# Optimization experiments

Measured on AMD Instinct MI355X. Metric: run time of the kernel, lower is better.

Reference implementation:

```python
import jax, jax.numpy as jnp
import numpy as np

EPS = 1e-10
BIG = 1e10

def setup_inputs() -> dict:
    key = jax.random.key(0)
    ks = jax.random.split(key, 8)
    B, N, D, H = 8, 2048, 128, 128
    K = 1434  # ceil(0.7 * N)
    X = jax.random.normal(ks[0], (B, N, D), dtype=jnp.float32)
    adj = jax.random.uniform(ks[1], (B, N, N), dtype=jnp.float32)
    mask = jnp.ones((B, N), dtype=jnp.float32)
    top_index = jax.random.randint(ks[2], (B, K), 0, N)
    # GCN params (xavier-normal-ish weights, zero bias)
    W1 = jax.random.normal(ks[3], (D, H), dtype=jnp.float32) * np.sqrt(2.0 / (D + H))
    b1 = jnp.zeros((H,), dtype=jnp.float32)
    W2 = jax.random.normal(ks[4], (H, H), dtype=jnp.float32) * np.sqrt(2.0 / (H + H))
    b2 = jnp.zeros((H,), dtype=jnp.float32)
    w_b = jax.random.uniform(ks[5], (1, H, 1), dtype=jnp.float32, minval=-1.0, maxval=1.0)
    tau = jnp.asarray(1.0, dtype=jnp.float32)
    return {"X": X, "adj": adj, "mask": mask, "W1": W1, "b1": b1,
            "W2": W2, "b2": b2, "w_b": w_b, "tau": tau, "top_index": top_index}

def reference(X, adj, mask, W1, b1, W2, b2, w_b, tau, top_index):
    # --- stacked GCN layers: relu((adj @ x) @ W + b) ---
    h = jax.nn.relu(jnp.matmul(jnp.matmul(adj, X), W1) + b1)
    h = jax.nn.relu(jnp.matmul(jnp.matmul(adj, h), W2) + b2)
    hidden = mask[:, :, None] * h  # [B,N,H]

    # --- neighbor-softmax attention (softmax == 'neibor') ---
    att_b = jnp.matmul(hidden, w_b)[..., 0] + (mask - 1.0) * BIG  # [B,N]
    att_b = jnp.exp((att_b - jnp.max(att_b, axis=1, keepdims=True)) * jnp.abs(tau))
    denom = jnp.einsum('bnm,bm->bn', adj, att_b) + EPS  # khop=1
    diag = jnp.diagonal(adj, axis1=1, axis2=2)  # [B,N]
    att_b = att_b * diag / denom
    att_b = att_b * jnp.sum(adj, axis=1)  # dnorm, adj_norm='none'
    att = att_b * mask

    Z = att[:, :, None] * hidden  # [B,N,H]

    # --- pooling via sampled top_index (full mask => k_list[i]==k_max) ---
    assign_m = jnp.take_along_axis(adj, top_index[:, :, None], axis=1)  # [B,K,N]
    assign_m = assign_m / (jnp.sum(assign_m, axis=1, keepdims=True) + EPS)
    H_out = jnp.matmul(assign_m, Z)  # [B,K,H]
    new_adj = jnp.matmul(jnp.matmul(assign_m, adj), jnp.swapaxes(assign_m, 1, 2))  # [B,K,K]
    new_mask = jnp.ones((X.shape[0], top_index.shape[1]), dtype=X.dtype)

    # mean pool readout
    out = jnp.sum(mask[:, :, None] * hidden, axis=1) / jnp.sum(mask, axis=1, keepdims=True)
    return out, H_out, new_adj, new_mask
```

## Files before the change

### kernel.cpp

```cpp
#include <hip/hip_runtime.h>
#include <hip/hip_bf16.h>

namespace {

constexpr int Bb = 8;
constexpr int Nn = 2048;
constexpr int Hh = 128;
constexpr int Kp = 1434;
constexpr int KpPad = 1536;
constexpr float kEps = 1e-10f;
constexpr float kBig = 1e10f;

using bf16x8 = __attribute__((ext_vector_type(8))) short;
using f32x4  = __attribute__((ext_vector_type(4))) float;

__device__ __forceinline__ float bf2f(unsigned u) {
  union { float f; unsigned q; } x; x.q = u << 16; return x.f;
}

__device__ __forceinline__ unsigned short f2bfbits(float f) {
  __hip_bfloat16 h = __float2bfloat16(f);
  return *reinterpret_cast<unsigned short*>(&h);
}

template<typename TA>
__device__ __forceinline__ void load8(const TA* p, float v[8]) {
  const float4* q = reinterpret_cast<const float4*>(p);
  float4 x0 = q[0], x1 = q[1];
  v[0]=x0.x; v[1]=x0.y; v[2]=x0.z; v[3]=x0.w;
  v[4]=x1.x; v[5]=x1.y; v[6]=x1.z; v[7]=x1.w;
}

template<typename TC>
__device__ __forceinline__ TC cvt_out(float v) {
  if constexpr (sizeof(TC) == 2) {
    return __float2bfloat16(v);
  } else {
    return v;
  }
}

__device__ __forceinline__ void gload_lds16(const void* g, void* l) {
  __builtin_amdgcn_global_load_lds(
      (const __attribute__((address_space(1))) void*)g,
      (__attribute__((address_space(3))) void*)l, 16, 0, 0);
}

template<typename TC>
__global__ __launch_bounds__(256, 4)
void mgemm_k(const __hip_bfloat16* __restrict__ A, long lda, long sA,
             const __hip_bfloat16* __restrict__ Bt, long ldb, long sB,
             const int* __restrict__ ag, int ag_stride, int Mg,
             const int* __restrict__ bg, int bg_stride, int Ng,
             TC* __restrict__ C, long ldc, long sC,
             int Ms, int Ns, int Kd)
{
  __shared__ char smem[32768];
  char* smA = smem;
  char* smB = smem + 16384;
  const int t = threadIdx.x;

  const int gx = gridDim.x, gy = gridDim.y;
  const int nwg = gx * gy * (int)gridDim.z;
  int lin = ((int)blockIdx.z * gy + (int)blockIdx.y) * gx + (int)blockIdx.x;
  lin = (lin & 7) * (nwg >> 3) + (lin >> 3);
  const int bx = lin % gx;
  const int by = (lin / gx) % gy;
  const int b  = lin / (gx * gy);

  const int m0 = by * 128, n0 = bx * 128;
  const int lane = t & 63, w = t >> 6;
  const int wr = w >> 1, wc = w & 1;

  const __hip_bfloat16* Ab = A + (size_t)b * sA;
  const __hip_bfloat16* Bb_ = Bt + (size_t)b * sB;

  const int srow = t >> 3;
  const int scol = ((t & 7) ^ (srow & 7)) * 16;
  const char* gA[4]; const char* gB[4];
#pragma unroll
  for (int q = 0; q < 4; ++q) {
    const int rowq = q * 32 + srow;
    long ga = m0 + rowq;
    if (ag) ga = (ga < Mg) ? (long)ag[(size_t)b * ag_stride + ga] : 0;
    gA[q] = (const char*)(Ab + ga * lda) + scol;
    long gb = n0 + rowq;
    if (bg) gb = (gb < Ng) ? (long)bg[(size_t)b * bg_stride + gb] : 0;
    gB[q] = (const char*)(Bb_ + gb * ldb) + scol;
  }

  f32x4 acc[4][4] = {};
  const int fr = lane & 15, kg = lane >> 4, fx = lane & 7;

  for (int kk = 0; kk < Kd; kk += 64) {
    __syncthreads();
#pragma unroll
    for (int q = 0; q < 4; ++q) {
      gload_lds16(gA[q] + (size_t)kk * 2, smA + q * 4096 + t * 16);
      gload_lds16(gB[q] + (size_t)kk * 2, smB + q * 4096 + t * 16);
    }
    __syncthreads();
#pragma unroll
    for (int ks = 0; ks < 2; ++ks) {
      bf16x8 aF[4], bF[4];
      const int slotbase = kg | (ks << 2);
#pragma unroll
      for (int mi = 0; mi < 4; ++mi) {
        const int off = (wr * 64 + mi * 16 + fr) * 128 + ((slotbase ^ fx) << 4);
        aF[mi] = *(const bf16x8*)(smA + off);
      }
#pragma unroll
      for (int ni = 0; ni < 4; ++ni) {
        const int off = (wc * 64 + ni * 16 + fr) * 128 + ((slotbase ^ fx) << 4);
        bF[ni] = *(const bf16x8*)(smB + off);
      }
#pragma unroll
      for (int mi = 0; mi < 4; ++mi)
#pragma unroll
        for (int ni = 0; ni < 4; ++ni)
          acc[mi][ni] = __builtin_amdgcn_mfma_f32_16x16x32_bf16(
              aF[mi], bF[ni], acc[mi][ni], 0, 0, 0);
    }
  }

  const int crow0 = m0 + wr * 64 + (lane >> 4) * 4;
  const int ccol0 = n0 + wc * 64 + fr;
#pragma unroll
  for (int mi = 0; mi < 4; ++mi) {
#pragma unroll
    for (int r = 0; r < 4; ++r) {
      const int row = crow0 + mi * 16 + r;
      if (row >= Ms) continue;
#pragma unroll
      for (int ni = 0; ni < 4; ++ni) {
        const int col = ccol0 + ni * 16;
        if (col >= Ns) continue;
        C[(size_t)b * sC + (size_t)row * ldc + col] = cvt_out<TC>(acc[mi][ni][r]);
      }
    }
  }
}

template<bool GATHER>
__global__ __launch_bounds__(256, 3)
void mlayer2_k(const __hip_bfloat16* __restrict__ A, long lda, long sA,
               const __hip_bfloat16* __restrict__ Bhi,
               const __hip_bfloat16* __restrict__ Blo, long ldb, long sB,
               const int* __restrict__ ag, int ag_stride, int Mg,
               float* __restrict__ P, int Mpad, int Kchunk)
{
  __shared__ char smem[49152];
  char* smA   = smem;
  char* smBhi = smem + 16384;
  char* smBlo = smem + 32768;
  const int t = threadIdx.x;
  const int b = blockIdx.z;
  const int sk = blockIdx.x;
  const int m0 = blockIdx.y * 128;
  const int k0 = sk * Kchunk;
  const int lane = t & 63, w = t >> 6;
  const int wr = w >> 1, wc = w & 1;

  const int srow = t >> 3;
  const int scol = ((t & 7) ^ (srow & 7)) * 16;
  const char* gA[4]; const char* gBhi[4]; const char* gBlo[4];
#pragma unroll
  for (int q = 0; q < 4; ++q) {
    const int rowq = q * 32 + srow;
    long ga = m0 + rowq;
    if (GATHER) ga = (ga < Mg) ? (long)ag[(size_t)b * ag_stride + ga] : 0;
    gA[q]   = (const char*)(A + (size_t)b * sA + ga * lda + k0) + scol;
    gBhi[q] = (const char*)(Bhi + (size_t)b * sB + (size_t)rowq * ldb + k0) + scol;
    gBlo[q] = (const char*)(Blo + (size_t)b * sB + (size_t)rowq * ldb + k0) + scol;
  }

  f32x4 acc[4][4] = {};
  const int fr = lane & 15, kg = lane >> 4, fx = lane & 7;

  for (int ks = 0; ks < Kchunk; ks += 64) {
    __syncthreads();
#pragma unroll
    for (int q = 0; q < 4; ++q) {
      gload_lds16(gA[q]   + (size_t)ks * 2, smA   + q * 4096 + t * 16);
      gload_lds16(gBhi[q] + (size_t)ks * 2, smBhi + q * 4096 + t * 16);
      gload_lds16(gBlo[q] + (size_t)ks * 2, smBlo + q * 4096 + t * 16);
    }
    __syncthreads();
#pragma unroll
    for (int ks2 = 0; ks2 < 2; ++ks2) {
      bf16x8 aF[4];
      const int slotbase = kg | (ks2 << 2);
#pragma unroll
      for (int mi = 0; mi < 4; ++mi) {
        const int off = (wr * 64 + mi * 16 + fr) * 128 + ((slotbase ^ fx) << 4);
        aF[mi] = *(const bf16x8*)(smA + off);
      }
#pragma unroll
      for (int ni = 0; ni < 4; ++ni) {
        const int off = (wc * 64 + ni * 16 + fr) * 128 + ((slotbase ^ fx) << 4);
        const bf16x8 bhi = *(const bf16x8*)(smBhi + off);
        const bf16x8 blo = *(const bf16x8*)(smBlo + off);
#pragma unroll
        for (int mi = 0; mi < 4; ++mi) {
          acc[mi][ni] = __builtin_amdgcn_mfma_f32_16x16x32_bf16(aF[mi], bhi, acc[mi][ni], 0, 0, 0);
          acc[mi][ni] = __builtin_amdgcn_mfma_f32_16x16x32_bf16(aF[mi], blo, acc[mi][ni], 0, 0, 0);
        }
      }
    }
  }

  float* Pp = P + ((size_t)sk * Bb + b) * Mpad * 128;
  const int crow0 = m0 + wr * 64 + (lane >> 4) * 4;
  const int ccol0 = wc * 64 + fr;
#pragma unroll
  for (int mi = 0; mi < 4; ++mi)
#pragma unroll
    for (int r = 0; r < 4; ++r) {
      const int row = crow0 + mi * 16 + r;
#pragma unroll
      for (int ni = 0; ni < 4; ++ni)
        Pp[(size_t)row * 128 + ccol0 + ni * 16] = acc[mi][ni][r];
    }
}

template<bool MASKED>
__global__ __launch_bounds__(256)
void red_layer_k(const float* __restrict__ P, const float* __restrict__ bias,
                 const float* __restrict__ mask, float* __restrict__ out)
{
  const size_t o = ((size_t)blockIdx.x * 256 + threadIdx.x) * 4;
  const size_t stride = (size_t)Bb * Nn * Hh;
  float4 s = {0.f, 0.f, 0.f, 0.f};
#pragma unroll
  for (int sk = 0; sk < 8; ++sk) {
    const float4 v = *(const float4*)(P + sk * stride + o);
    s.x += v.x; s.y += v.y; s.z += v.z; s.w += v.w;
  }
  const int h = (int)(o & 127);
  const float4 bi = *(const float4*)(bias + h);
  s.x = fmaxf(s.x + bi.x, 0.f);
  s.y = fmaxf(s.y + bi.y, 0.f);
  s.z = fmaxf(s.z + bi.z, 0.f);
  s.w = fmaxf(s.w + bi.w, 0.f);
  if (MASKED) {
    const int n = (int)((o >> 7) & (Nn - 1));
    const int b = (int)(o >> 18);
    const float m = mask[b * Nn + n];
    s.x *= m; s.y *= m; s.z *= m; s.w *= m;
  }
  *(float4*)(out + o) = s;
}

__global__ __launch_bounds__(128)
void red_hout_k(const float* __restrict__ P, float* __restrict__ Hout)
{
  const int k = blockIdx.x, b = blockIdx.y, h = threadIdx.x;
  const size_t stride = (size_t)Bb * KpPad * Hh;
  float s = 0.f;
#pragma unroll
  for (int sk = 0; sk < 8; ++sk)
    s += P[sk * stride + ((size_t)b * KpPad + k) * 128 + h];
  Hout[((size_t)b * Kp + k) * 128 + h] = s;
}

__global__ __launch_bounds__(256)
void wgemm_k(const float* __restrict__ A, long sA,
             const float* __restrict__ W,
             float* __restrict__ Cp)
{
  __shared__ float As[16][128];
  __shared__ float Bs[16][128];
  const int tid = threadIdx.x;
  const int p = blockIdx.x;
  const int b = blockIdx.z;
  const int m0 = blockIdx.y * 128;
  const int k0 = p * 64;
  const int ty = tid >> 4, tx = tid & 15;

  const float* Ab = A + (size_t)b * sA;

  float acc[8][8];
#pragma unroll
  for (int r = 0; r < 8; ++r)
#pragma unroll
    for (int c = 0; c < 8; ++c) acc[r][c] = 0.f;

  const int ai = tid >> 1;
  const int ak0 = (tid & 1) * 8;

  for (int kk0 = k0; kk0 < k0 + 64; kk0 += 16) {
    float av[8];
    load8<float>(Ab + (size_t)(m0 + ai) * Hh + kk0 + ak0, av);
    float bv[8];
    const int bk_row = tid >> 4, bj0 = (tid & 15) * 8;
    load8<float>(W + (size_t)(kk0 + bk_row) * Hh + bj0, bv);

    __syncthreads();
#pragma unroll
    for (int e = 0; e < 8; ++e) Bs[bk_row][bj0 + e] = bv[e];
#pragma unroll
    for (int e = 0; e < 8; ++e) As[ak0 + e][ai] = av[e];
    __syncthreads();

#pragma unroll
    for (int k = 0; k < 16; ++k) {
      const float4 a0 = *reinterpret_cast<const float4*>(&As[k][4 * ty]);
      const float4 a1 = *reinterpret_cast<const float4*>(&As[k][64 + 4 * ty]);
      const float4 b0 = *reinterpret_cast<const float4*>(&Bs[k][4 * tx]);
      const float4 b1 = *reinterpret_cast<const float4*>(&Bs[k][64 + 4 * tx]);
      const float ar[8] = {a0.x, a0.y, a0.z, a0.w, a1.x, a1.y, a1.z, a1.w};
      const float br[8] = {b0.x, b0.y, b0.z, b0.w, b1.x, b1.y, b1.z, b1.w};
#pragma unroll
      for (int r = 0; r < 8; ++r)
#pragma unroll
        for (int c = 0; c < 8; ++c)
          acc[r][c] = fmaf(ar[r], br[c], acc[r][c]);
    }
  }

  float* Cb = Cp + (size_t)p * Bb * Nn * Hh + (size_t)b * sA;
#pragma unroll
  for (int r = 0; r < 8; ++r) {
    const int gi = m0 + ((r < 4) ? (4 * ty + r) : (64 + 4 * ty + r - 4));
#pragma unroll
    for (int c = 0; c < 8; ++c) {
      const int gj = (c < 4) ? (4 * tx + c) : (64 + 4 * tx + c - 4);
      Cb[(size_t)gi * Hh + gj] = acc[r][c];
    }
  }
}


__global__ __launch_bounds__(256)
void prep_k(const float* __restrict__ adj, const float* __restrict__ invc,
            __hip_bfloat16* __restrict__ S, __hip_bfloat16* __restrict__ At,
            float* __restrict__ pa)
{
  __shared__ float tile[32][36];
  const int b = blockIdx.z;
  const long j0 = (long)blockIdx.x * 32;
  const long ibase = (long)blockIdx.y * 64;
  const int r = threadIdx.x >> 3, c4 = (threadIdx.x & 7) * 4;
  const float4 ic = *(const float4*)(invc + (size_t)b * Nn + j0 + c4);
  float cs = 0.f;
#pragma unroll
  for (int st = 0; st < 2; ++st) {
    const long i0 = ibase + st * 32;
    const float4 v = *(const float4*)(adj + ((size_t)b * Nn + (i0 + r)) * Nn + j0 + c4);
    ushort4 sv;
    sv.x = f2bfbits(v.x * ic.x);
    sv.y = f2bfbits(v.y * ic.y);
    sv.z = f2bfbits(v.z * ic.z);
    sv.w = f2bfbits(v.w * ic.w);
    *(ushort4*)((unsigned short*)S + ((size_t)b * Nn + (i0 + r)) * Nn + j0 + c4) = sv;
    tile[r][c4 + 0] = v.x;
    tile[r][c4 + 1] = v.y;
    tile[r][c4 + 2] = v.z;
    tile[r][c4 + 3] = v.w;
    __syncthreads();
    ushort4 tv;
    tv.x = f2bfbits(tile[c4 + 0][r]);
    tv.y = f2bfbits(tile[c4 + 1][r]);
    tv.z = f2bfbits(tile[c4 + 2][r]);
    tv.w = f2bfbits(tile[c4 + 3][r]);
    *(ushort4*)((unsigned short*)At + ((size_t)b * Nn + (j0 + r)) * Nn + i0 + c4) = tv;
    if (threadIdx.x < 32) {
      float a = 0.f;
#pragma unroll
      for (int rr = 0; rr < 32; ++rr) a += tile[rr][threadIdx.x];
      cs += a;
    }
    __syncthreads();
  }
  if (threadIdx.x < 32)
    pa[(((size_t)b * 32 + blockIdx.y) << 11) + j0 + threadIdx.x] = cs;
}

__global__ __launch_bounds__(256)
void tconv2_k(const float* __restrict__ p0, const float* __restrict__ p1,
              long ld_src, long s_src,
              const float* __restrict__ scale, long scale_stride,
              __hip_bfloat16* __restrict__ dst, __hip_bfloat16* __restrict__ dlo,
              long ld_dst, long s_dst)
{
  __shared__ float tile[32][36];
  const int b = blockIdx.z;
  const long i0 = (long)blockIdx.y * 32, j0 = (long)blockIdx.x * 32;
  const int r = threadIdx.x >> 3, c4 = (threadIdx.x & 7) * 4;
  const size_t soff = (size_t)b * s_src + (i0 + r) * ld_src + j0 + c4;
  float4 v = *(const float4*)(p0 + soff);
  if (p1) {
    const float4 u = *(const float4*)(p1 + soff);
    v.x += u.x; v.y += u.y; v.z += u.z; v.w += u.w;
  }
  const float sc = scale[(size_t)b * scale_stride + i0 + r];
  tile[r][c4 + 0] = v.x * sc;
  tile[r][c4 + 1] = v.y * sc;
  tile[r][c4 + 2] = v.z * sc;
  tile[r][c4 + 3] = v.w * sc;
  __syncthreads();
  float t0 = tile[c4 + 0][r], t1 = tile[c4 + 1][r], t2 = tile[c4 + 2][r], t3 = tile[c4 + 3][r];
  ushort4 hi;
  hi.x = f2bfbits(t0); hi.y = f2bfbits(t1); hi.z = f2bfbits(t2); hi.w = f2bfbits(t3);
  const size_t doff = (size_t)b * s_dst + (j0 + r) * ld_dst + i0 + c4;
  *(ushort4*)((unsigned short*)dst + doff) = hi;
  ushort4 lo;
  lo.x = f2bfbits(t0 - bf2f(hi.x));
  lo.y = f2bfbits(t1 - bf2f(hi.y));
  lo.z = f2bfbits(t2 - bf2f(hi.z));
  lo.w = f2bfbits(t3 - bf2f(hi.w));
  *(ushort4*)((unsigned short*)dlo + doff) = lo;
}


__global__ __launch_bounds__(256)
void colsum_c_part_k(const float* __restrict__ adj, const int* __restrict__ top,
                     float* __restrict__ pc)
{
  __shared__ int rows[180];
  const int b = blockIdx.z, ch = blockIdx.y;
  const int n = blockIdx.x * 256 + threadIdx.x;
  const int k0 = ch * 180;
  const int cnt = min(Kp - k0, 180);
  for (int k = threadIdx.x; k < cnt; k += 256) rows[k] = top[b * Kp + k0 + k];
  __syncthreads();
  const float* ab = adj + (size_t)b * Nn * Nn;
  float a0 = 0.f, a1 = 0.f, a2 = 0.f, a3 = 0.f;
  int k = 0;
  for (; k + 4 <= cnt; k += 4) {
    a0 += ab[(size_t)rows[k + 0] * Nn + n];
    a1 += ab[(size_t)rows[k + 1] * Nn + n];
    a2 += ab[(size_t)rows[k + 2] * Nn + n];
    a3 += ab[(size_t)rows[k + 3] * Nn + n];
  }
  for (; k < cnt; ++k) a0 += ab[(size_t)rows[k] * Nn + n];
  pc[(((size_t)b * 8 + ch) << 11) + n] = (a0 + a1) + (a2 + a3);
}

__global__ __launch_bounds__(256)
void invc_fin_k(const float* __restrict__ pc, float* __restrict__ invc,
                float* __restrict__ cvec)
{
  const int i = blockIdx.x * 256 + threadIdx.x;
  const int b = i >> 11, n = i & (Nn - 1);
  float s = 0.f;
#pragma unroll
  for (int ch = 0; ch < 8; ++ch) s += pc[(((size_t)b * 8 + ch) << 11) + n];
  const float c = s + kEps;
  cvec[i] = c;
  invc[i] = 1.f / c;
}

__global__ __launch_bounds__(256)
void csum_fin_k(const float* __restrict__ pa, float* __restrict__ csum)
{
  const int i = blockIdx.x * 256 + threadIdx.x;
  const int b = i >> 11, m = i & (Nn - 1);
  float s = 0.f;
#pragma unroll
  for (int ch = 0; ch < 32; ++ch) s += pa[(((size_t)b * 32 + ch) << 11) + m];
  csum[i] = s;
}

__global__ __launch_bounds__(256)
void denom2_k(const __hip_bfloat16* __restrict__ S, const float* __restrict__ ca,
              const float* __restrict__ cvec,
              float* __restrict__ denom, float* __restrict__ diag)
{
  const int b = blockIdx.y;
  const int w = threadIdx.x >> 6, lane = threadIdx.x & 63;
  const int n = blockIdx.x * 4 + w;
  const unsigned short* srow = (const unsigned short*)S + ((size_t)b * Nn + n) * Nn;
  const float* cap = ca + (size_t)b * Nn;
  float acc = 0.f;
#pragma unroll
  for (int j = 0; j < 4; ++j) {
    const int o = j * 512 + lane * 8;
    const uint4 u = *(const uint4*)(srow + o);
    const float4 c0 = *(const float4*)(cap + o);
    const float4 c1 = *(const float4*)(cap + o + 4);
    acc += bf2f(u.x & 0xffffu) * c0.x + bf2f(u.x >> 16) * c0.y
         + bf2f(u.y & 0xffffu) * c0.z + bf2f(u.y >> 16) * c0.w
         + bf2f(u.z & 0xffffu) * c1.x + bf2f(u.z >> 16) * c1.y
         + bf2f(u.w & 0xffffu) * c1.z + bf2f(u.w >> 16) * c1.w;
  }
#pragma unroll
  for (int o = 32; o; o >>= 1) acc += __shfl_down(acc, o, 64);
  if (lane == 0) {
    denom[(size_t)b * Nn + n] = acc;
    diag[(size_t)b * Nn + n] = bf2f(srow[n]) * cvec[(size_t)b * Nn + n];
  }
}

__global__ __launch_bounds__(128)
void readout_part_k(const float* __restrict__ hid, const float* __restrict__ mask,
                    float* __restrict__ rp)
{
  const int b = blockIdx.y, ch = blockIdx.x, h = threadIdx.x;
  const float* hp = hid + ((size_t)b * Nn + ch * 128) * Hh;
  const float* mp = mask + (size_t)b * Nn + ch * 128;
  float acc = 0.f;
#pragma unroll 1
  for (int r = 0; r < 128; ++r) acc += mp[r] * hp[(size_t)r * Hh + h];
  rp[(((size_t)b * 16 + ch) << 7) + h] = acc;
}

__global__ __launch_bounds__(128)
void readout_fin_k(const float* __restrict__ rp, const float* __restrict__ mask,
                   float* __restrict__ out)
{
  __shared__ float sm[128];
  const int b = blockIdx.x, h = threadIdx.x;
  float acc = 0.f;
#pragma unroll
  for (int ch = 0; ch < 16; ++ch) acc += rp[(((size_t)b * 16 + ch) << 7) + h];
  float ms = 0.f;
#pragma unroll
  for (int j = 0; j < 16; ++j) ms += mask[(size_t)b * Nn + h * 16 + j];
  sm[h] = ms;
  __syncthreads();
  for (int o = 64; o; o >>= 1) {
    if (h < o) sm[h] += sm[h + o];
    __syncthreads();
  }
  out[(size_t)b * Hh + h] = acc / sm[0];
}


__global__ __launch_bounds__(256)
void scores_k(const float* __restrict__ hidden, const float* __restrict__ wb,
              const float* __restrict__ mask, float* __restrict__ s)
{
  const int wid = threadIdx.x >> 6, lane = threadIdx.x & 63;
  const int row = blockIdx.x * 4 + wid;
  const float* hp = hidden + (size_t)row * Hh;
  float acc = hp[lane] * wb[lane] + hp[64 + lane] * wb[64 + lane];
#pragma unroll
  for (int o = 32; o; o >>= 1) acc += __shfl_down(acc, o, 64);
  if (lane == 0) s[row] = acc + (mask[row] - 1.f) * kBig;
}

__global__ __launch_bounds__(256)
void rowmax_k(const float* __restrict__ s, float* __restrict__ rmax)
{
  __shared__ float red[256];
  const int b = blockIdx.x;
  float m = -3.4e38f;
  for (int n = threadIdx.x; n < Nn; n += 256) m = fmaxf(m, s[b * Nn + n]);
  red[threadIdx.x] = m;
  __syncthreads();
  for (int o = 128; o; o >>= 1) {
    if (threadIdx.x < o) red[threadIdx.x] = fmaxf(red[threadIdx.x], red[threadIdx.x + o]);
    __syncthreads();
  }
  if (threadIdx.x == 0) rmax[b] = red[0];
}

__global__ __launch_bounds__(256)
void attexp_k(const float* __restrict__ s, const float* __restrict__ rmax,
              const float* __restrict__ tau, const float* __restrict__ cvec,
              float* __restrict__ atte, float* __restrict__ ca)
{
  const int i = blockIdx.x * 256 + threadIdx.x;
  const int b = i >> 11;
  const float e = expf((s[i] - rmax[b]) * fabsf(*tau));
  atte[i] = e;
  ca[i] = e * cvec[i];
}

__global__ __launch_bounds__(256)
void att_final_k(const float* __restrict__ atte, const float* __restrict__ diag,
                 const float* __restrict__ denom, const float* __restrict__ colsum,
                 const float* __restrict__ mask, float* __restrict__ att)
{
  const int i = blockIdx.x * 256 + threadIdx.x;
  att[i] = atte[i] * diag[i] / (denom[i] + kEps) * colsum[i] * mask[i];
}

__global__ __launch_bounds__(256)
void ones_k(float* __restrict__ p, int n)
{
  const int i = blockIdx.x * 256 + threadIdx.x;
  if (i < n) p[i] = 1.f;
}

}

extern "C" void kernel_launch(void* const* d_in, const int* in_sizes, int n_in,
                              void* d_out, int out_size, void* d_ws, size_t ws_size,
                              hipStream_t stream) {
  const float* X    = (const float*)d_in[0];
  const float* adj  = (const float*)d_in[1];
  const float* mask = (const float*)d_in[2];
  const float* W1   = (const float*)d_in[3];
  const float* b1   = (const float*)d_in[4];
  const float* W2   = (const float*)d_in[5];
  const float* b2   = (const float*)d_in[6];
  const float* wb   = (const float*)d_in[7];
  const float* tau  = (const float*)d_in[8];
  const int*   top  = (const int*)d_in[9];
  float* out = (float*)d_out;

  float* ws    = (float*)d_ws;
  float* h1hid = ws;
  float* Btf   = ws + 2097152;
  float* invc  = ws + 4194304;
  float* cvec  = ws + 4210688;
  float* s     = ws + 4227072;
  float* atte  = ws + 4243456;
  float* den   = ws + 4259840;
  float* diag  = ws + 4276224;
  float* csum  = ws + 4292608;
  float* att   = ws + 4308992;
  float* ca    = ws + 4325376;
  float* rmax  = ws + 4341760;
  float* pc    = ws + 4342016;
  float* pa    = ws + 4473088;
  float* rp    = ws + 4997376;
  __hip_bfloat16* S   = (__hip_bfloat16*)(ws + 5013760);
  __hip_bfloat16* At  = S + (size_t)Bb * Nn * Nn;
  float*          P   = (float*)At;
  __hip_bfloat16* T   = At + (size_t)Bb * Nn * Nn;
  float*          Tpart = (float*)T;
  if (ws_size < 204604416u) return;

  __hip_bfloat16* Bthi = (__hip_bfloat16*)Btf;
  __hip_bfloat16* Btlo = Bthi + (size_t)Bb * Hh * Nn;

  float* Hout    = out + 1024;
  float* newadj  = out + 1469440;
  float* newmask = out + 17920288;

  const long sAdj = (long)Nn * Nn;
  const long sNH  = (long)Nn * Hh;
  const long sHN  = (long)Hh * Nn;
  const long sT   = (long)KpPad * Nn;
  const long sNew = (long)Kp * Kp;

  colsum_c_part_k<<<dim3(Nn / 256, 8, Bb), 256, 0, stream>>>(adj, top, pc);
  invc_fin_k<<<dim3(Bb * Nn / 256), 256, 0, stream>>>(pc, invc, cvec);

  prep_k<<<dim3(Nn / 32, Nn / 64, Bb), 256, 0, stream>>>(adj, invc, S, At, pa);
  csum_fin_k<<<dim3(Bb * Nn / 256), 256, 0, stream>>>(pa, csum);

  mgemm_k<__hip_bfloat16><<<dim3(Nn / 128, KpPad / 128, Bb), 256, 0, stream>>>(
      S, Nn, sAdj, At, Nn, sAdj, top, Kp, Kp, nullptr, 0, 0,
      T, Nn, sT, KpPad, Nn, Nn);
  mgemm_k<float><<<dim3(KpPad / 128, KpPad / 128, Bb), 256, 0, stream>>>(
      T, Nn, sT, S, Nn, sAdj, nullptr, 0, 0, top, Kp, Kp,
      newadj, Kp, sNew, Kp, Kp, Nn);

  wgemm_k<<<dim3(2, Nn / 128, Bb), 256, 0, stream>>>(X, sNH, W1, Tpart);
  tconv2_k<<<dim3(Hh / 32, Nn / 32, Bb), 256, 0, stream>>>(
      Tpart, Tpart + (size_t)Bb * Nn * Hh, Hh, sNH, cvec, Nn, Bthi, Btlo, Nn, sHN);
  mlayer2_k<false><<<dim3(8, Nn / 128, Bb), 256, 0, stream>>>(
      S, Nn, sAdj, Bthi, Btlo, Nn, sHN, nullptr, 0, 0, P, Nn, Nn / 8);
  red_layer_k<false><<<dim3(2048), 256, 0, stream>>>(P, b1, nullptr, h1hid);

  wgemm_k<<<dim3(2, Nn / 128, Bb), 256, 0, stream>>>(h1hid, sNH, W2, Tpart);
  tconv2_k<<<dim3(Hh / 32, Nn / 32, Bb), 256, 0, stream>>>(
      Tpart, Tpart + (size_t)Bb * Nn * Hh, Hh, sNH, cvec, Nn, Bthi, Btlo, Nn, sHN);
  mlayer2_k<false><<<dim3(8, Nn / 128, Bb), 256, 0, stream>>>(
      S, Nn, sAdj, Bthi, Btlo, Nn, sHN, nullptr, 0, 0, P, Nn, Nn / 8);
  red_layer_k<true><<<dim3(2048), 256, 0, stream>>>(P, b2, mask, h1hid);

  scores_k<<<dim3(Bb * Nn / 4), 256, 0, stream>>>(h1hid, wb, mask, s);
  rowmax_k<<<dim3(Bb), 256, 0, stream>>>(s, rmax);
  attexp_k<<<dim3(Bb * Nn / 256), 256, 0, stream>>>(s, rmax, tau, cvec, atte, ca);
  denom2_k<<<dim3(Nn / 4, Bb), 256, 0, stream>>>(S, ca, cvec, den, diag);
  att_final_k<<<dim3(Bb * Nn / 256), 256, 0, stream>>>(atte, diag, den, csum, mask, att);

  tconv2_k<<<dim3(Hh / 32, Nn / 32, Bb), 256, 0, stream>>>(
      h1hid, nullptr, Hh, sNH, att, Nn, Bthi, Btlo, Nn, sHN);
  mlayer2_k<true><<<dim3(8, KpPad / 128, Bb), 256, 0, stream>>>(
      S, Nn, sAdj, Bthi, Btlo, Nn, sHN, top, Kp, Kp, P, KpPad, Nn / 8);
  red_hout_k<<<dim3(Kp, Bb), 128, 0, stream>>>(P, Hout);

  readout_part_k<<<dim3(16, Bb), 128, 0, stream>>>(h1hid, mask, rp);
  readout_fin_k<<<dim3(Bb), 128, 0, stream>>>(rp, mask, out);
  ones_k<<<dim3((Bb * Kp + 255) / 256), 256, 0, stream>>>(newmask, Bb * Kp);
}
```

Measured before the change: 502.0 us.

## Switch GEMMs to 32x32x16 MFMA and halve split-K factor in layer kernels

Both the mgemm and mlayer2 kernels replace 16x16x32 bf16 MFMA tiles with 32x32x16 MFMA tiles, with matching fragment indexing and epilogue. The larger instruction shape means fewer LDS fragment reads per FLOP and fewer MFMA issues. Separately, the split-K factor for the layer GEMMs drops from 8 to 4 (Kchunk doubled), so the reduction kernels read half as many partials. The catch is fewer blocks per launch, which means less parallelism, and the epilogue writes with a different access pattern.

```diff
diff --git a/kernel.cpp b/kernel.cpp
--- a/kernel.cpp
+++ b/kernel.cpp
@@ -13,6 +13,7 @@
 
 using bf16x8 = __attribute__((ext_vector_type(8))) short;
 using f32x4  = __attribute__((ext_vector_type(4))) float;
+using f32x16 = __attribute__((ext_vector_type(16))) float;
 
 __device__ __forceinline__ float bf2f(unsigned u) {
   union { float f; unsigned q; } x; x.q = u << 16; return x.f;
@@ -89,8 +90,8 @@
     gB[q] = (const char*)(Bb_ + gb * ldb) + scol;
   }
 
-  f32x4 acc[4][4] = {};
-  const int fr = lane & 15, kg = lane >> 4, fx = lane & 7;
+  f32x16 acc[2][2] = {};
+  const int l31 = lane & 31, kh = lane >> 5, fx = lane & 7;
 
   for (int kk = 0; kk < Kd; kk += 64) {
     __syncthreads();
@@ -101,40 +102,38 @@
     }
     __syncthreads();
 #pragma unroll
-    for (int ks = 0; ks < 2; ++ks) {
-      bf16x8 aF[4], bF[4];
-      const int slotbase = kg | (ks << 2);
-#pragma unroll
-      for (int mi = 0; mi < 4; ++mi) {
-        const int off = (wr * 64 + mi * 16 + fr) * 128 + ((slotbase ^ fx) << 4);
-        aF[mi] = *(const bf16x8*)(smA + off);
+    for (int ks2 = 0; ks2 < 4; ++ks2) {
+      const int slotk = ks2 * 2 + kh;
+      bf16x8 aF[2], bF[2];
+#pragma unroll
+      for (int mi = 0; mi < 2; ++mi) {
+        const int row = wr * 64 + mi * 32 + l31;
+        aF[mi] = *(const bf16x8*)(smA + row * 128 + ((slotk ^ fx) << 4));
       }
 #pragma unroll
-      for (int ni = 0; ni < 4; ++ni) {
-        const int off = (wc * 64 + ni * 16 + fr) * 128 + ((slotbase ^ fx) << 4);
-        bF[ni] = *(const bf16x8*)(smB + off);
+      for (int ni = 0; ni < 2; ++ni) {
+        const int row = wc * 64 + ni * 32 + l31;
+        bF[ni] = *(const bf16x8*)(smB + row * 128 + ((slotk ^ fx) << 4));
       }
 #pragma unroll
-      for (int mi = 0; mi < 4; ++mi)
-#pragma unroll
-        for (int ni = 0; ni < 4; ++ni)
-          acc[mi][ni] = __builtin_amdgcn_mfma_f32_16x16x32_bf16(
+      for (int mi = 0; mi < 2; ++mi)
+#pragma unroll
+        for (int ni = 0; ni < 2; ++ni)
+          acc[mi][ni] = __builtin_amdgcn_mfma_f32_32x32x16_bf16(
               aF[mi], bF[ni], acc[mi][ni], 0, 0, 0);
     }
   }
 
-  const int crow0 = m0 + wr * 64 + (lane >> 4) * 4;
-  const int ccol0 = n0 + wc * 64 + fr;
-#pragma unroll
-  for (int mi = 0; mi < 4; ++mi) {
-#pragma unroll
-    for (int r = 0; r < 4; ++r) {
-      const int row = crow0 + mi * 16 + r;
-      if (row >= Ms) continue;
-#pragma unroll
-      for (int ni = 0; ni < 4; ++ni) {
-        const int col = ccol0 + ni * 16;
-        if (col >= Ns) continue;
+#pragma unroll
+  for (int mi = 0; mi < 2; ++mi) {
+#pragma unroll
+    for (int ni = 0; ni < 2; ++ni) {
+      const int col = n0 + wc * 64 + ni * 32 + l31;
+      if (col >= Ns) continue;
+#pragma unroll
+      for (int r = 0; r < 16; ++r) {
+        const int row = m0 + wr * 64 + mi * 32 + (r & 3) + 8 * (r >> 2) + 4 * kh;
+        if (row >= Ms) continue;
         C[(size_t)b * sC + (size_t)row * ldc + col] = cvt_out<TC>(acc[mi][ni][r]);
       }
     }
@@ -174,8 +173,8 @@
     gBlo[q] = (const char*)(Blo + (size_t)b * sB + (size_t)rowq * ldb + k0) + scol;
   }
 
-  f32x4 acc[4][4] = {};
-  const int fr = lane & 15, kg = lane >> 4, fx = lane & 7;
+  f32x16 acc[2][2] = {};
+  const int l31 = lane & 31, kh = lane >> 5, fx = lane & 7;
 
   for (int ks = 0; ks < Kchunk; ks += 64) {
     __syncthreads();
@@ -187,40 +186,41 @@
     }
     __syncthreads();
 #pragma unroll
-    for (int ks2 = 0; ks2 < 2; ++ks2) {
-      bf16x8 aF[4];
-      const int slotbase = kg | (ks2 << 2);
-#pragma unroll
-      for (int mi = 0; mi < 4; ++mi) {
-        const int off = (wr * 64 + mi * 16 + fr) * 128 + ((slotbase ^ fx) << 4);
-        aF[mi] = *(const bf16x8*)(smA + off);
+    for (int ks2 = 0; ks2 < 4; ++ks2) {
+      const int slotk = ks2 * 2 + kh;
+      bf16x8 aF[2];
+#pragma unroll
+      for (int mi = 0; mi < 2; ++mi) {
+        const int row = wr * 64 + mi * 32 + l31;
+        aF[mi] = *(const bf16x8*)(smA + row * 128 + ((slotk ^ fx) << 4));
       }
 #pragma unroll
-      for (int ni = 0; ni < 4; ++ni) {
-        const int off = (wc * 64 + ni * 16 + fr) * 128 + ((slotbase ^ fx) << 4);
-        const bf16x8 bhi = *(const bf16x8*)(smBhi + off);
-        const bf16x8 blo = *(const bf16x8*)(smBlo + off);
-#pragma unroll
-        for (int mi = 0; mi < 4; ++mi) {
-          acc[mi][ni] = __builtin_amdgcn_mfma_f32_16x16x32_bf16(aF[mi], bhi, acc[mi][ni], 0, 0, 0);
-          acc[mi][ni] = __builtin_amdgcn_mfma_f32_16x16x32_bf16(aF[mi], blo, acc[mi][ni], 0, 0, 0);
+      for (int ni = 0; ni < 2; ++ni) {
+        const int row = wc * 64 + ni * 32 + l31;
+        const bf16x8 bhi = *(const bf16x8*)(smBhi + row * 128 + ((slotk ^ fx) << 4));
+        const bf16x8 blo = *(const bf16x8*)(smBlo + row * 128 + ((slotk ^ fx) << 4));
+#pragma unroll
+        for (int mi = 0; mi < 2; ++mi) {
+          acc[mi][ni] = __builtin_amdgcn_mfma_f32_32x32x16_bf16(aF[mi], bhi, acc[mi][ni], 0, 0, 0);
+          acc[mi][ni] = __builtin_amdgcn_mfma_f32_32x32x16_bf16(aF[mi], blo, acc[mi][ni], 0, 0, 0);
         }
       }
     }
   }
 
   float* Pp = P + ((size_t)sk * Bb + b) * Mpad * 128;
-  const int crow0 = m0 + wr * 64 + (lane >> 4) * 4;
-  const int ccol0 = wc * 64 + fr;
-#pragma unroll
-  for (int mi = 0; mi < 4; ++mi)
-#pragma unroll
-    for (int r = 0; r < 4; ++r) {
-      const int row = crow0 + mi * 16 + r;
-#pragma unroll
-      for (int ni = 0; ni < 4; ++ni)
-        Pp[(size_t)row * 128 + ccol0 + ni * 16] = acc[mi][ni][r];
-    }
+#pragma unroll
+  for (int mi = 0; mi < 2; ++mi) {
+#pragma unroll
+    for (int ni = 0; ni < 2; ++ni) {
+      const int col = wc * 64 + ni * 32 + l31;
+#pragma unroll
+      for (int r = 0; r < 16; ++r) {
+        const int row = m0 + wr * 64 + mi * 32 + (r & 3) + 8 * (r >> 2) + 4 * kh;
+        Pp[(size_t)row * 128 + col] = acc[mi][ni][r];
+      }
+    }
+  }
 }
 
 template<bool MASKED>
@@ -232,7 +232,7 @@
   const size_t stride = (size_t)Bb * Nn * Hh;
   float4 s = {0.f, 0.f, 0.f, 0.f};
 #pragma unroll
-  for (int sk = 0; sk < 8; ++sk) {
+  for (int sk = 0; sk < 4; ++sk) {
     const float4 v = *(const float4*)(P + sk * stride + o);
     s.x += v.x; s.y += v.y; s.z += v.z; s.w += v.w;
   }
@@ -258,7 +258,7 @@
   const size_t stride = (size_t)Bb * KpPad * Hh;
   float s = 0.f;
 #pragma unroll
-  for (int sk = 0; sk < 8; ++sk)
+  for (int sk = 0; sk < 4; ++sk)
     s += P[sk * stride + ((size_t)b * KpPad + k) * 128 + h];
   Hout[((size_t)b * Kp + k) * 128 + h] = s;
 }
@@ -653,15 +653,15 @@
   wgemm_k<<<dim3(2, Nn / 128, Bb), 256, 0, stream>>>(X, sNH, W1, Tpart);
   tconv2_k<<<dim3(Hh / 32, Nn / 32, Bb), 256, 0, stream>>>(
       Tpart, Tpart + (size_t)Bb * Nn * Hh, Hh, sNH, cvec, Nn, Bthi, Btlo, Nn, sHN);
-  mlayer2_k<false><<<dim3(8, Nn / 128, Bb), 256, 0, stream>>>(
-      S, Nn, sAdj, Bthi, Btlo, Nn, sHN, nullptr, 0, 0, P, Nn, Nn / 8);
+  mlayer2_k<false><<<dim3(4, Nn / 128, Bb), 256, 0, stream>>>(
+      S, Nn, sAdj, Bthi, Btlo, Nn, sHN, nullptr, 0, 0, P, Nn, Nn / 4);
   red_layer_k<false><<<dim3(2048), 256, 0, stream>>>(P, b1, nullptr, h1hid);
 
   wgemm_k<<<dim3(2, Nn / 128, Bb), 256, 0, stream>>>(h1hid, sNH, W2, Tpart);
   tconv2_k<<<dim3(Hh / 32, Nn / 32, Bb), 256, 0, stream>>>(
       Tpart, Tpart + (size_t)Bb * Nn * Hh, Hh, sNH, cvec, Nn, Bthi, Btlo, Nn, sHN);
-  mlayer2_k<false><<<dim3(8, Nn / 128, Bb), 256, 0, stream>>>(
-      S, Nn, sAdj, Bthi, Btlo, Nn, sHN, nullptr, 0, 0, P, Nn, Nn / 8);
+  mlayer2_k<false><<<dim3(4, Nn / 128, Bb), 256, 0, stream>>>(
+      S, Nn, sAdj, Bthi, Btlo, Nn, sHN, nullptr, 0, 0, P, Nn, Nn / 4);
   red_layer_k<true><<<dim3(2048), 256, 0, stream>>>(P, b2, mask, h1hid);
 
   scores_k<<<dim3(Bb * Nn / 4), 256, 0, stream>>>(h1hid, wb, mask, s);
@@ -672,8 +672,8 @@
 
   tconv2_k<<<dim3(Hh / 32, Nn / 32, Bb), 256, 0, stream>>>(
       h1hid, nullptr, Hh, sNH, att, Nn, Bthi, Btlo, Nn, sHN);
-  mlayer2_k<true><<<dim3(8, KpPad / 128, Bb), 256, 0, stream>>>(
-      S, Nn, sAdj, Bthi, Btlo, Nn, sHN, top, Kp, Kp, P, KpPad, Nn / 8);
+  mlayer2_k<true><<<dim3(4, KpPad / 128, Bb), 256, 0, stream>>>(
+      S, Nn, sAdj, Bthi, Btlo, Nn, sHN, top, Kp, Kp, P, KpPad, Nn / 4);
   red_hout_k<<<dim3(Kp, Bb), 128, 0, stream>>>(P, Hout);
 
   readout_part_k<<<dim3(16, Bb), 128, 0, stream>>>(h1hid, mask, rp);
```

New measurement: 519.0 us. +3.4%, slower.
